# Kernel optimization log

Measured on AMD Instinct MI355X. Metric: run time of the kernel, lower is better.

## Reference

```python
import jax, jax.numpy as jnp
import numpy as np

EPS = 1e-7  # K.epsilon()
ROUTINGS = 3


def squash(v, axis=-1):
    s2 = jnp.sum(jnp.square(v), axis=axis, keepdims=True)
    scale = s2 / (1.0 + s2) / jnp.sqrt(s2 + EPS)
    return scale * v


def setup_inputs() -> dict:
    key = jax.random.key(0)
    k1, k2 = jax.random.split(key)
    B, I, D, O, K = 64, 2048, 8, 32, 16
    x = jax.random.normal(k1, (B, I, D), dtype=jnp.float32)
    W = jax.random.normal(k2, (I, O, D, K), dtype=jnp.float32) * 0.05
    return {"x": x, "W": W}


def reference(x, W):
    # u_hat[b,o,i,k] = sum_d x[b,i,d] * W[i,o,d,k]
    u_hat = jnp.einsum('bid,iodk->boik', x, W)  # [B, O, I, K]
    B, O, I, _ = u_hat.shape
    b = jnp.zeros((B, O, I), dtype=u_hat.dtype)
    v = None
    for i in range(ROUTINGS):
        c = jax.nn.softmax(b, axis=1)                      # over output capsules
        s = jnp.einsum('boi,boik->bok', c, u_hat)          # weighted sum
        v = squash(s)                                      # [B, O, K]
        if i < ROUTINGS - 1:
            agreement = jnp.einsum('boik,bok->boi', u_hat, v)
            b = b + agreement
    return v
```

## Files before the change

### kernel.cpp

```cpp
#include <hip/hip_runtime.h>


__device__ __forceinline__ float4 f4add(float4 a, float4 b) {
    return make_float4(a.x + b.x, a.y + b.y, a.z + b.z, a.w + b.w);
}
__device__ __forceinline__ int swz(int f4) { return f4 ^ ((f4 >> 3) & 7); }

template<int PASS0>
__global__ __launch_bounds__(512, 4)
void pass_kernel(const float* __restrict__ x,
                 const float* __restrict__ W,
                 const float* __restrict__ vin,
                 float* __restrict__ part)
{
    __shared__ __align__(16) float x_lds[32 * 64];
    __shared__ __align__(16) float red[8 * 2 * 512];
    __shared__ __align__(16) float vg[2 * 512];

    const int t  = threadIdx.x;
    const int w  = t >> 6;
    const int l  = t & 63;
    const int o  = l & 31;
    const int kk = l >> 5;
    const int bx = blockIdx.x;
    const int ch = bx & 255;
    const int h  = bx >> 8;
    const int i  = ch * 8 + w;

    const int f4a = swz(o * 4 + kk * 2);
    const int f4b = swz(o * 4 + kk * 2 + 1);

    float Wr[8][8];
    {
        const float* wp = W + (size_t)(i * 32 + o) * 128 + kk * 8;
        #pragma unroll
        for (int d = 0; d < 8; ++d) {
            float4 a = *(const float4*)(wp + d * 16);
            float4 b = *(const float4*)(wp + d * 16 + 4);
            Wr[d][0] = a.x; Wr[d][1] = a.y; Wr[d][2] = a.z; Wr[d][3] = a.w;
            Wr[d][4] = b.x; Wr[d][5] = b.y; Wr[d][6] = b.z; Wr[d][7] = b.w;
        }
        #pragma unroll
        for (int d = 0; d < 8; ++d)
            #pragma unroll
            for (int j = 0; j < 8; ++j)
                asm volatile("" : "+v"(Wr[d][j]));
    }
    {
        const int f  = t * 4;
        const int bl = f >> 6, r = f & 63;
        *(float4*)&x_lds[f] =
            *(const float4*)(x + (size_t)(h * 32 + bl) * 16384 + ch * 64 + r);
    }

    for (int g = 0; g < 16; ++g) {
        if (!PASS0) {
            if (t < 256) {
                const int bq = t >> 7, idx = t & 127;
                const int b  = h * 32 + g * 2 + bq;
                *(float4*)&vg[(bq * 128 + swz(idx)) * 4] =
                    *(const float4*)(vin + (size_t)b * 512 + idx * 4);
            }
        }
        __syncthreads();

        #pragma unroll
        for (int bq = 0; bq < 2; ++bq) {
            const int bl = g * 2 + bq;
            float4 xa = *(const float4*)&x_lds[bl * 64 + w * 8];
            float4 xb = *(const float4*)&x_lds[bl * 64 + w * 8 + 4];
            float xr[8] = {xa.x, xa.y, xa.z, xa.w, xb.x, xb.y, xb.z, xb.w};
            float uh[8];
            #pragma unroll
            for (int j = 0; j < 8; ++j) uh[j] = 0.f;
            #pragma unroll
            for (int d = 0; d < 8; ++d) {
                #pragma unroll
                for (int j = 0; j < 8; ++j)
                    uh[j] = fmaf(xr[d], Wr[d][j], uh[j]);
            }
            float c;
            if (PASS0) {
                c = 0.03125f;
            } else {
                const float4 va = *(const float4*)&vg[(bq * 128 + f4a) * 4];
                const float4 vb = *(const float4*)&vg[(bq * 128 + f4b) * 4];
                float logit = uh[0] * va.x;
                logit = fmaf(uh[1], va.y, logit);
                logit = fmaf(uh[2], va.z, logit);
                logit = fmaf(uh[3], va.w, logit);
                logit = fmaf(uh[4], vb.x, logit);
                logit = fmaf(uh[5], vb.y, logit);
                logit = fmaf(uh[6], vb.z, logit);
                logit = fmaf(uh[7], vb.w, logit);
                logit += __shfl_xor(logit, 32, 64);
                float ex = __expf(logit);
                float sm = ex;
                #pragma unroll
                for (int off = 16; off >= 1; off >>= 1)
                    sm += __shfl_xor(sm, off, 64);
                c = __fdividef(ex, sm);
            }
            const int rb = (w * 2 + bq) * 128;
            *(float4*)&red[(rb + f4a) * 4] =
                make_float4(c * uh[0], c * uh[1], c * uh[2], c * uh[3]);
            *(float4*)&red[(rb + f4b) * 4] =
                make_float4(c * uh[4], c * uh[5], c * uh[6], c * uh[7]);
        }
        __syncthreads();

        if (t < 256) {
            const int bq = t >> 7, j4 = t & 127;
            const int sj = swz(j4);
            float4 s = make_float4(0.f, 0.f, 0.f, 0.f);
            #pragma unroll
            for (int slot = 0; slot < 8; ++slot)
                s = f4add(s, *(const float4*)&red[((slot * 2 + bq) * 128 + sj) * 4]);
            const int b = h * 32 + g * 2 + bq;
            *(float4*)(part + ((size_t)b * 256 + ch) * 512 + j4 * 4) = s;
        }
    }
}

template<int PHASE>
__global__ __launch_bounds__(1024)
void reduce_kernel(const float* __restrict__ part,
                   float* __restrict__ vsum,
                   float* __restrict__ out)
{
    __shared__ float sred[16 * 64];
    const int bx = blockIdx.x;
    const int b  = bx >> 3;
    const int q  = bx & 7;
    const int t  = threadIdx.x;
    const int e  = t & 63;
    const int p  = t >> 6;

    const float* p0 = part + ((size_t)b * 256 + p) * 512 + q * 64 + e;
    float acc = 0.f;
    #pragma unroll
    for (int cc = 0; cc < 16; ++cc)
        acc += p0[(size_t)cc * 16 * 512];
    sred[p * 64 + e] = acc;
    __syncthreads();

    if (t < 64) {
        float s = 0.f;
        #pragma unroll
        for (int pp = 0; pp < 16; ++pp)
            s += sred[pp * 64 + t];
        float sq = s * s;
        #pragma unroll
        for (int off = 8; off >= 1; off >>= 1)
            sq += __shfl_xor(sq, off, 16);
        float v = (sq / (1.f + sq) * rsqrtf(sq + 1e-7f)) * s;
        const size_t idx = (size_t)b * 512 + q * 64 + t;
        if (PHASE == 2)      out[idx]   = v;
        else if (PHASE == 1) vsum[idx] += v;
        else                 vsum[idx]  = v;
    }
}

extern "C" void kernel_launch(void* const* d_in, const int* in_sizes, int n_in,
                              void* d_out, int out_size, void* d_ws, size_t ws_size,
                              hipStream_t stream)
{
    const float* x = (const float*)d_in[0];
    const float* W = (const float*)d_in[1];
    float* out = (float*)d_out;
    char* ws = (char*)d_ws;

    const size_t partB = (size_t)64 * 256 * 512 * 4;
    const size_t vsumB = (size_t)64 * 512 * 4;
    if (ws_size < partB + vsumB) return;

    float* part = (float*)ws;
    float* vsum = (float*)(ws + partB);

    pass_kernel<1><<<512, 512, 0, stream>>>(x, W, vsum, part);
    reduce_kernel<0><<<512, 1024, 0, stream>>>(part, vsum, out);
    pass_kernel<0><<<512, 512, 0, stream>>>(x, W, vsum, part);
    reduce_kernel<1><<<512, 1024, 0, stream>>>(part, vsum, out);
    pass_kernel<0><<<512, 512, 0, stream>>>(x, W, vsum, part);
    reduce_kernel<2><<<512, 1024, 0, stream>>>(part, vsum, out);
}
```

Baseline: 196.7 us.

## Double-buffer LDS reduction, load v directly from global, vectorize reduce kernel

The pass kernel now double-buffers its per-warp partial LDS buffer, so the cross-warp reduction of step g-1 runs after the barrier at the start of step g. This removes one __syncthreads per iteration and spreads the reduction across all 512 threads using float2. The v vector is read straight from global memory (L1/L2 cached) instead of being staged through LDS. The reduce kernel uses float4 loads with a two-level LDS reduction to reach higher memory throughput. The trade-offs are roughly twice the LDS footprint, which may lower occupancy, and more global loads of v.

```diff
diff --git a/kernel.cpp b/kernel.cpp
--- a/kernel.cpp
+++ b/kernel.cpp
@@ -14,8 +14,7 @@
                  float* __restrict__ part)
 {
     __shared__ __align__(16) float x_lds[32 * 64];
-    __shared__ __align__(16) float red[8 * 2 * 512];
-    __shared__ __align__(16) float vg[2 * 512];
+    __shared__ __align__(16) float red[2][16 * 512];
 
     const int t  = threadIdx.x;
     const int w  = t >> 6;
@@ -29,6 +28,9 @@
 
     const int f4a = swz(o * 4 + kk * 2);
     const int f4b = swz(o * 4 + kk * 2 + 1);
+    const int bqf = t >> 8;
+    const int j2  = t & 255;
+    const int sjf = swz(j2 >> 1) * 4 + (j2 & 1) * 2;
 
     float Wr[8][8];
     {
@@ -53,20 +55,32 @@
             *(const float4*)(x + (size_t)(h * 32 + bl) * 16384 + ch * 64 + r);
     }
 
+    #pragma unroll 2
     for (int g = 0; g < 16; ++g) {
-        if (!PASS0) {
-            if (t < 256) {
-                const int bq = t >> 7, idx = t & 127;
-                const int b  = h * 32 + g * 2 + bq;
-                *(float4*)&vg[(bq * 128 + swz(idx)) * 4] =
-                    *(const float4*)(vin + (size_t)b * 512 + idx * 4);
-            }
-        }
         __syncthreads();
 
+        if (g) {
+            const float* rp = red[(g - 1) & 1];
+            float2 s = make_float2(0.f, 0.f);
+            #pragma unroll
+            for (int slot = 0; slot < 8; ++slot) {
+                const float2 v = *(const float2*)&rp[(slot * 2 + bqf) * 512 + sjf];
+                s.x += v.x; s.y += v.y;
+            }
+            const int b = h * 32 + (g - 1) * 2 + bqf;
+            *(float2*)(part + ((size_t)b * 256 + ch) * 512 + j2 * 2) = s;
+        }
+
+        float* rw = red[g & 1];
         #pragma unroll
         for (int bq = 0; bq < 2; ++bq) {
             const int bl = g * 2 + bq;
+            float4 va, vb;
+            if (!PASS0) {
+                const float* vp = vin + (size_t)(h * 32 + bl) * 512 + o * 16 + kk * 8;
+                va = *(const float4*)vp;
+                vb = *(const float4*)(vp + 4);
+            }
             float4 xa = *(const float4*)&x_lds[bl * 64 + w * 8];
             float4 xb = *(const float4*)&x_lds[bl * 64 + w * 8 + 4];
             float xr[8] = {xa.x, xa.y, xa.z, xa.w, xb.x, xb.y, xb.z, xb.w};
@@ -83,8 +97,6 @@
             if (PASS0) {
                 c = 0.03125f;
             } else {
-                const float4 va = *(const float4*)&vg[(bq * 128 + f4a) * 4];
-                const float4 vb = *(const float4*)&vg[(bq * 128 + f4b) * 4];
                 float logit = uh[0] * va.x;
                 logit = fmaf(uh[1], va.y, logit);
                 logit = fmaf(uh[2], va.z, logit);
@@ -101,24 +113,23 @@
                     sm += __shfl_xor(sm, off, 64);
                 c = __fdividef(ex, sm);
             }
-            const int rb = (w * 2 + bq) * 128;
-            *(float4*)&red[(rb + f4a) * 4] =
+            *(float4*)&rw[((w * 2 + bq) * 128 + f4a) * 4] =
                 make_float4(c * uh[0], c * uh[1], c * uh[2], c * uh[3]);
-            *(float4*)&red[(rb + f4b) * 4] =
+            *(float4*)&rw[((w * 2 + bq) * 128 + f4b) * 4] =
                 make_float4(c * uh[4], c * uh[5], c * uh[6], c * uh[7]);
         }
-        __syncthreads();
-
-        if (t < 256) {
-            const int bq = t >> 7, j4 = t & 127;
-            const int sj = swz(j4);
-            float4 s = make_float4(0.f, 0.f, 0.f, 0.f);
-            #pragma unroll
-            for (int slot = 0; slot < 8; ++slot)
-                s = f4add(s, *(const float4*)&red[((slot * 2 + bq) * 128 + sj) * 4]);
-            const int b = h * 32 + g * 2 + bq;
-            *(float4*)(part + ((size_t)b * 256 + ch) * 512 + j4 * 4) = s;
-        }
+    }
+    __syncthreads();
+    {
+        const float* rp = red[1];
+        float2 s = make_float2(0.f, 0.f);
+        #pragma unroll
+        for (int slot = 0; slot < 8; ++slot) {
+            const float2 v = *(const float2*)&rp[(slot * 2 + bqf) * 512 + sjf];
+            s.x += v.x; s.y += v.y;
+        }
+        const int b = h * 32 + 15 * 2 + bqf;
+        *(float2*)(part + ((size_t)b * 256 + ch) * 512 + j2 * 2) = s;
     }
 }
 
@@ -128,32 +139,39 @@
                    float* __restrict__ vsum,
                    float* __restrict__ out)
 {
-    __shared__ float sred[16 * 64];
+    __shared__ __align__(16) float4 sred[64][16];
+    __shared__ __align__(16) float4 sredB[16][16];
     const int bx = blockIdx.x;
     const int b  = bx >> 3;
     const int q  = bx & 7;
     const int t  = threadIdx.x;
-    const int e  = t & 63;
-    const int p  = t >> 6;
-
-    const float* p0 = part + ((size_t)b * 256 + p) * 512 + q * 64 + e;
-    float acc = 0.f;
-    #pragma unroll
-    for (int cc = 0; cc < 16; ++cc)
-        acc += p0[(size_t)cc * 16 * 512];
-    sred[p * 64 + e] = acc;
+    const int f  = t & 15;
+    const int c0 = t >> 4;
+
+    const float4* p4 =
+        (const float4*)(part + ((size_t)b * 256 + c0) * 512 + q * 64) + f;
+    float4 s = f4add(f4add(p4[0],          p4[64 * 128]),
+                     f4add(p4[128 * 128],  p4[192 * 128]));
+    sred[c0][f] = s;
     __syncthreads();
 
+    if (t < 256) {
+        const int fr = t & 15, r = t >> 4;
+        sredB[r][fr] = f4add(f4add(sred[r][fr],      sred[r + 16][fr]),
+                             f4add(sred[r + 32][fr], sred[r + 48][fr]));
+    }
+    __syncthreads();
+
     if (t < 64) {
-        float s = 0.f;
-        #pragma unroll
-        for (int pp = 0; pp < 16; ++pp)
-            s += sred[pp * 64 + t];
-        float sq = s * s;
+        const float* sB = (const float*)sredB;
+        float s1 = 0.f;
+        #pragma unroll
+        for (int r = 0; r < 16; ++r) s1 += sB[r * 64 + t];
+        float sq = s1 * s1;
         #pragma unroll
         for (int off = 8; off >= 1; off >>= 1)
             sq += __shfl_xor(sq, off, 16);
-        float v = (sq / (1.f + sq) * rsqrtf(sq + 1e-7f)) * s;
+        float v = (sq / (1.f + sq) * rsqrtf(sq + 1e-7f)) * s1;
         const size_t idx = (size_t)b * 512 + q * 64 + t;
         if (PHASE == 2)      out[idx]   = v;
         else if (PHASE == 1) vsum[idx] += v;
```

After: 191.9 us. 1.02x faster.
